# Kernel tuning notes

Measured on AMD Instinct MI355X. Metric: run time of the kernel, lower is better.

The kernel has to match this reference:

```python
import jax, jax.numpy as jnp
import numpy as np

D_MODEL = 1024
NUM_HEADS = 16
D_K = D_MODEL // NUM_HEADS


def setup_inputs() -> dict:
    key = jax.random.key(0)
    ks = jax.random.split(key, 9)
    B, S = 2, 2048
    s_in = 1.0 / np.sqrt(D_MODEL)
    x = jax.random.normal(ks[0], (B, S, D_MODEL), dtype=jnp.float32)
    # Linear weights stored as (in_features, out_features): y = x @ W + b
    Wq = jax.random.uniform(ks[1], (D_MODEL, D_MODEL), jnp.float32, -s_in, s_in)
    bq = jax.random.uniform(ks[2], (D_MODEL,), jnp.float32, -s_in, s_in)
    Wk = jax.random.uniform(ks[3], (D_MODEL, D_K), jnp.float32, -s_in, s_in)
    bk = jax.random.uniform(ks[4], (D_K,), jnp.float32, -s_in, s_in)
    Wv = jax.random.uniform(ks[5], (D_MODEL, D_K), jnp.float32, -s_in, s_in)
    bv = jax.random.uniform(ks[6], (D_K,), jnp.float32, -s_in, s_in)
    Wo = jax.random.uniform(ks[7], (D_MODEL, D_MODEL), jnp.float32, -s_in, s_in)
    bo = jax.random.uniform(ks[8], (D_MODEL,), jnp.float32, -s_in, s_in)
    return {"x": x, "Wq": Wq, "bq": bq, "Wk": Wk, "bk": bk,
            "Wv": Wv, "bv": bv, "Wo": Wo, "bo": bo}


def reference(x, Wq, bq, Wk, bk, Wv, bv, Wo, bo):
    B, S, _ = x.shape
    H, Dk = NUM_HEADS, D_K
    # Projections
    Q = (x @ Wq + bq).reshape(B, S, H, Dk).transpose(0, 2, 1, 3)  # [B,H,S,Dk]
    K = x @ Wk + bk                                               # [B,S,Dk] single KV head
    V = x @ Wv + bv                                               # [B,S,Dk]
    # Scores: query heads broadcast against the single shared KV head
    scores = jnp.einsum('bhqd,bkd->bhqk', Q, K) / jnp.sqrt(jnp.float32(Dk))
    attn = jax.nn.softmax(scores, axis=-1)                        # [B,H,S,S]
    out = jnp.einsum('bhqk,bkd->bhqd', attn, V)                   # [B,H,S,Dk]
    out = out.transpose(0, 2, 1, 3).reshape(B, S, H * Dk)         # [B,S,d_model]
    return out @ Wo + bo
```

## Files before the change

kernel.cpp:

```cpp
#include <hip/hip_runtime.h>
#include <hip/hip_bf16.h>

typedef __attribute__((ext_vector_type(8))) short bf16x8;
typedef __attribute__((ext_vector_type(4))) float f32x4;
typedef __attribute__((ext_vector_type(16))) float f32x16;
typedef __attribute__((ext_vector_type(4))) unsigned short ushort4v;

#define QSCALE 0.1803368801111204f

__device__ __forceinline__ unsigned short f2bf(float f) {
  union { float f; unsigned int u; } x; x.f = f;
  unsigned int u = x.u;
  unsigned int r = (u + 0x7fffu + ((u >> 16) & 1u)) >> 16;
  return (unsigned short)r;
}

__device__ __forceinline__ unsigned short cvt1bf(float a) {
  union { __hip_bfloat162 h; unsigned short s[2]; } c;
  c.h = __float22bfloat162_rn(make_float2(a, a));
  return c.s[0];
}

__device__ __forceinline__ void gll16(const unsigned short* g, unsigned short* l) {
  __builtin_amdgcn_global_load_lds(
      (const __attribute__((address_space(1))) unsigned int*)g,
      (__attribute__((address_space(3))) unsigned int*)l, 16, 0, 0);
}

__global__ __launch_bounds__(256) void prep_kernel(
    const float* __restrict__ x,
    const float* __restrict__ Wq, const float* __restrict__ Wk,
    const float* __restrict__ Wv, const float* __restrict__ Wo,
    unsigned short* __restrict__ xb,
    unsigned short* __restrict__ QKVt, unsigned short* __restrict__ Wot) {
  int z = blockIdx.z;
  if (z == 4) {
    size_t base = ((size_t)(blockIdx.y * 32 + blockIdx.x)) * 4096 + threadIdx.x * 16;
#pragma unroll
    for (int c = 0; c < 4; ++c) {
      float4 v = *(const float4*)(x + base + c * 4);
      ushort4v o = { f2bf(v.x), f2bf(v.y), f2bf(v.z), f2bf(v.w) };
      *(ushort4v*)(xb + base + c * 4) = o;
    }
    return;
  }
  __shared__ float t[32][33];
  const float* src;
  unsigned short* dst;
  int C, rowoff;
  if (z == 0)      { src = Wq; dst = QKVt; C = 1024; rowoff = 0; }
  else if (z == 1) { src = Wk; dst = QKVt; C = 64;   rowoff = 1024; }
  else if (z == 2) { src = Wv; dst = QKVt; C = 64;   rowoff = 1088; }
  else             { src = Wo; dst = Wot;  C = 1024; rowoff = 0; }
  int c0 = blockIdx.x * 32, r0 = blockIdx.y * 32;
  if (c0 >= C) return;
  int tx = threadIdx.x & 31, ty = threadIdx.x >> 5;
#pragma unroll
  for (int i = 0; i < 32; i += 8)
    t[ty + i][tx] = src[(size_t)(r0 + ty + i) * C + c0 + tx];
  __syncthreads();
#pragma unroll
  for (int i = 0; i < 32; i += 8)
    dst[(size_t)(rowoff + c0 + ty + i) * 1024 + r0 + tx] = f2bf(t[tx][ty + i]);
}

template <typename OutT, bool QKVMODE>
__global__ __launch_bounds__(256) void gemm_bf16_kernel(
    const unsigned short* __restrict__ A, const unsigned short* __restrict__ Bt,
    const float* __restrict__ b0, const float* __restrict__ b1,
    const float* __restrict__ b2, OutT* __restrict__ C,
    unsigned short* __restrict__ Vt, int M, int N, int K) {
  __shared__ __align__(16) unsigned short As[2][128 * 32];
  __shared__ __align__(16) unsigned short Bs[2][64 * 32];
  int tid = threadIdx.x;
  int wid = tid >> 6, lane = tid & 63;
  int l15 = lane & 15, quad = lane >> 4;
  int m0 = blockIdx.x * 128, n0 = blockIdx.y * 64;
  int mw = (wid >> 1) * 64, nw = (wid & 1) * 32;
  f32x4 acc[4][2];
#pragma unroll
  for (int i = 0; i < 4; i++)
#pragma unroll
    for (int j = 0; j < 2; j++)
#pragma unroll
      for (int e = 0; e < 4; ++e) acc[i][j][e] = 0.f;

  const unsigned short* Ag = A + (size_t)(m0 + (tid >> 2)) * K + (tid & 3) * 8;
  const unsigned short* Bg = Bt + (size_t)(n0 + (tid >> 2)) * K + (tid & 3) * 8;

  gll16(Ag, As[0] + tid * 8);
  gll16(Ag + (size_t)64 * K, As[0] + 2048 + tid * 8);
  gll16(Bg, Bs[0] + tid * 8);

  for (int k0 = 0; k0 < K; k0 += 32) {
    int cur = (k0 >> 5) & 1;
    if (k0 + 32 < K) {
      int nxt = cur ^ 1;
      gll16(Ag + k0 + 32, As[nxt] + tid * 8);
      gll16(Ag + (size_t)64 * K + k0 + 32, As[nxt] + 2048 + tid * 8);
      gll16(Bg + k0 + 32, Bs[nxt] + tid * 8);
      asm volatile("s_waitcnt vmcnt(3)" ::: "memory");
    } else {
      asm volatile("s_waitcnt vmcnt(0)" ::: "memory");
    }
    __builtin_amdgcn_s_barrier();
    __builtin_amdgcn_sched_barrier(0);
    const unsigned short* Asb = As[cur];
    const unsigned short* Bsb = Bs[cur];
    bf16x8 af[4], bfr[2];
#pragma unroll
    for (int t = 0; t < 4; ++t)
      af[t] = *(const bf16x8*)(Asb + (mw + t * 16 + l15) * 32 + quad * 8);
#pragma unroll
    for (int t = 0; t < 2; ++t)
      bfr[t] = *(const bf16x8*)(Bsb + (nw + t * 16 + l15) * 32 + quad * 8);
#pragma unroll
    for (int mt = 0; mt < 4; ++mt)
#pragma unroll
      for (int nt = 0; nt < 2; ++nt)
        acc[mt][nt] = __builtin_amdgcn_mfma_f32_16x16x32_bf16(
            af[mt], bfr[nt], acc[mt][nt], 0, 0, 0);
    asm volatile("s_waitcnt lgkmcnt(0)" ::: "memory");
    __builtin_amdgcn_sched_barrier(0);
    __builtin_amdgcn_s_barrier();
  }
#pragma unroll
  for (int mt = 0; mt < 4; ++mt)
#pragma unroll
    for (int nt = 0; nt < 2; ++nt) {
      int col = n0 + nw + nt * 16 + l15;
      float bias, cs;
      if constexpr (QKVMODE) {
        bias = (col < 1024) ? b0[col] : ((col < 1088) ? b1[col - 1024] : b2[col - 1088]);
        cs = (col < 1024) ? QSCALE : 1.0f;
      } else {
        bias = b0[col];
        cs = 1.0f;
      }
#pragma unroll
      for (int r = 0; r < 4; ++r) {
        int row = m0 + mw + mt * 16 + quad * 4 + r;
        float v = (acc[mt][nt][r] + bias) * cs;
        if constexpr (sizeof(OutT) == 2)
          C[(size_t)row * N + col] = f2bf(v);
        else
          C[(size_t)row * N + col] = v;
        if constexpr (QKVMODE) {
          if (col >= 1088)
            Vt[((size_t)(row >> 11) * 64 + (col - 1088)) * 2048 + (row & 2047)] =
                f2bf(v);
        }
      }
    }
}

__global__ __launch_bounds__(512, 4) void flash_attn_kernel(
    const unsigned short* __restrict__ QKV,
    const unsigned short* __restrict__ Vt,
    unsigned short* __restrict__ AO) {
  constexpr int S = 2048, LDQ = 1152;
  constexpr int PK = 72, PP = 72;
  __shared__ unsigned short Ks[2][64 * PK];
  __shared__ unsigned short Vs[2][64 * PK];
  __shared__ unsigned short Ps[8][32 * PP];
  int tid = threadIdx.x;
  int wid = tid >> 6, lane = tid & 63;
  int l31 = lane & 31, half = lane >> 5;
  int p = wid & 3, ks = wid >> 2;
  int q0 = blockIdx.x * 128, h = blockIdx.y, b = blockIdx.z;

  const unsigned short* Qb =
      QKV + (size_t)(b * S + q0 + p * 32 + l31) * LDQ + h * 64 + half * 8;
  bf16x8 qf[4];
#pragma unroll
  for (int f = 0; f < 4; ++f) qf[f] = *(const bf16x8*)(Qb + f * 16);

  int u = tid & 255, sl = tid >> 8;
  int srow = u >> 2, sc = (u & 3) * 8;
  const unsigned short* Kgb = QKV + ((size_t)b * S) * LDQ + 1024;
  const unsigned short* Vgb = Vt + ((size_t)(b * 64 + srow)) * 2048;

  f32x16 oa0, oa1;
#pragma unroll
  for (int r = 0; r < 16; ++r) { oa0[r] = 0.f; oa1[r] = 0.f; }
  float rs[16];
#pragma unroll
  for (int r = 0; r < 16; ++r) rs[r] = 0.f;

  int kb0 = sl * 1024;
  bf16x8 ka = *(const bf16x8*)(Kgb + (size_t)(kb0 + srow) * LDQ + sc);
  bf16x8 kc = *(const bf16x8*)(Kgb + (size_t)(kb0 + srow) * LDQ + sc + 32);
  bf16x8 va = *(const bf16x8*)(Vgb + kb0 + sc);
  bf16x8 vc = *(const bf16x8*)(Vgb + kb0 + sc + 32);

  unsigned short* Pw = Ps[wid];
  unsigned short* Ksb = Ks[ks];
  unsigned short* Vsb = Vs[ks];

  for (int kt = 0; kt < 16; ++kt) {
    *(bf16x8*)(Ks[sl] + srow * PK + sc) = ka;
    *(bf16x8*)(Ks[sl] + srow * PK + sc + 32) = kc;
    *(bf16x8*)(Vs[sl] + srow * PK + sc) = va;
    *(bf16x8*)(Vs[sl] + srow * PK + sc + 32) = vc;
    __syncthreads();
    if (kt + 1 < 16) {
      int kbn = sl * 1024 + (kt + 1) * 64;
      ka = *(const bf16x8*)(Kgb + (size_t)(kbn + srow) * LDQ + sc);
      kc = *(const bf16x8*)(Kgb + (size_t)(kbn + srow) * LDQ + sc + 32);
      va = *(const bf16x8*)(Vgb + kbn + sc);
      vc = *(const bf16x8*)(Vgb + kbn + sc + 32);
    }

#pragma unroll
    for (int n2 = 0; n2 < 2; ++n2) {
      f32x16 sacc;
#pragma unroll
      for (int i = 0; i < 16; ++i) sacc[i] = 0.f;
#pragma unroll
      for (int s = 0; s < 4; ++s) {
        bf16x8 kf =
            *(const bf16x8*)(Ksb + (n2 * 32 + l31) * PK + s * 16 + half * 8);
        sacc = __builtin_amdgcn_mfma_f32_32x32x16_bf16(qf[s], kf, sacc, 0, 0, 0);
      }
#pragma unroll
      for (int r = 0; r < 16; ++r) {
        float pr = __builtin_amdgcn_exp2f(sacc[r]);
        rs[r] += pr;
        int row = (r & 3) + 8 * (r >> 2) + 4 * half;
        Pw[row * PP + n2 * 32 + l31] = cvt1bf(pr);
      }
    }

    bf16x8 pf[4];
#pragma unroll
    for (int s = 0; s < 4; ++s)
      pf[s] = *(const bf16x8*)(Pw + l31 * PP + s * 16 + half * 8);
#pragma unroll
    for (int s = 0; s < 4; ++s) {
      bf16x8 vf0 = *(const bf16x8*)(Vsb + (l31)*PK + s * 16 + half * 8);
      bf16x8 vf1 = *(const bf16x8*)(Vsb + (32 + l31) * PK + s * 16 + half * 8);
      oa0 = __builtin_amdgcn_mfma_f32_32x32x16_bf16(pf[s], vf0, oa0, 0, 0, 0);
      oa1 = __builtin_amdgcn_mfma_f32_32x32x16_bf16(pf[s], vf1, oa1, 0, 0, 0);
    }
    __syncthreads();
  }

#pragma unroll
  for (int r = 0; r < 16; ++r) {
    float t = rs[r];
    t += __shfl_xor(t, 1, 32);
    t += __shfl_xor(t, 2, 32);
    t += __shfl_xor(t, 4, 32);
    t += __shfl_xor(t, 8, 32);
    t += __shfl_xor(t, 16, 32);
    rs[r] = t;
  }

  float* Cb = (float*)Ps;
  if (ks == 1) {
#pragma unroll
    for (int r = 0; r < 16; ++r) {
      int row = (r & 3) + 8 * (r >> 2) + 4 * half;
      Cb[(p * 32 + row) * 65 + l31] = oa0[r];
      Cb[(p * 32 + row) * 65 + 32 + l31] = oa1[r];
      if (l31 == 0) Cb[(p * 32 + row) * 65 + 64] = rs[r];
    }
  }
  __syncthreads();
  if (ks == 0) {
    unsigned short* Ob = AO + (size_t)(b * S + q0 + p * 32) * 1024 + h * 64;
#pragma unroll
    for (int r = 0; r < 16; ++r) {
      int row = (r & 3) + 8 * (r >> 2) + 4 * half;
      float p0 = Cb[(p * 32 + row) * 65 + l31];
      float p1 = Cb[(p * 32 + row) * 65 + 32 + l31];
      float rsu = Cb[(p * 32 + row) * 65 + 64];
      float inv = 1.0f / (rs[r] + rsu);
      Ob[(size_t)row * 1024 + l31] = f2bf((oa0[r] + p0) * inv);
      Ob[(size_t)row * 1024 + 32 + l31] = f2bf((oa1[r] + p1) * inv);
    }
  }
}

extern "C" void kernel_launch(void* const* d_in, const int* in_sizes, int n_in,
                              void* d_out, int out_size, void* d_ws, size_t ws_size,
                              hipStream_t stream) {
  const float* x  = (const float*)d_in[0];
  const float* Wq = (const float*)d_in[1];
  const float* bq = (const float*)d_in[2];
  const float* Wk = (const float*)d_in[3];
  const float* bk = (const float*)d_in[4];
  const float* Wv = (const float*)d_in[5];
  const float* bv = (const float*)d_in[6];
  const float* Wo = (const float*)d_in[7];
  const float* bo = (const float*)d_in[8];
  float* out = (float*)d_out;

  constexpr int B = 2, S = 2048, D = 1024, Dk = 64, H = 16;
  constexpr int M = B * S;
  constexpr int NQKV = D + 2 * Dk;

  char* ws = (char*)d_ws;
  unsigned short* xb   = (unsigned short*)ws; ws += (size_t)M * D * 2;
  unsigned short* QKVt = (unsigned short*)ws; ws += (size_t)NQKV * D * 2;
  unsigned short* Wot  = (unsigned short*)ws; ws += (size_t)D * D * 2;
  unsigned short* QKV  = (unsigned short*)ws; ws += (size_t)M * NQKV * 2;
  unsigned short* Vtb  = (unsigned short*)ws; ws += (size_t)B * Dk * S * 2;
  unsigned short* AO   = (unsigned short*)ws; ws += (size_t)M * D * 2;

  prep_kernel<<<dim3(32, 32, 5), 256, 0, stream>>>(x, Wq, Wk, Wv, Wo, xb, QKVt, Wot);

  gemm_bf16_kernel<unsigned short, true><<<dim3(M / 128, NQKV / 64), 256, 0, stream>>>(
      xb, QKVt, bq, bk, bv, QKV, Vtb, M, NQKV, D);

  flash_attn_kernel<<<dim3(S / 128, H, B), 512, 0, stream>>>(QKV, Vtb, AO);

  gemm_bf16_kernel<float, false><<<dim3(M / 128, D / 64), 256, 0, stream>>>(
      AO, Wot, bo, nullptr, nullptr, out, nullptr, M, D, D);
}
```

Baseline: 185.9 us.

## Triple-buffer GEMM with BK=64 and XOR-swizzled LDS layout

Reworks the projection GEMM main loop to stage K-tiles of 64 instead of 32, use three LDS buffers with a two-deep prefetch, and XOR-swizzle the LDS chunk layout to avoid bank conflicts on fragment reads. The aim is to hide more global-load latency and halve the barrier count per K. In exchange it raises LDS use to about 72KB per block, which may lower occupancy.

After: 192.6 us. 1.04x slower.

```diff
diff --git a/kernel.cpp b/kernel.cpp
--- a/kernel.cpp
+++ b/kernel.cpp
@@ -70,8 +70,8 @@
     const float* __restrict__ b0, const float* __restrict__ b1,
     const float* __restrict__ b2, OutT* __restrict__ C,
     unsigned short* __restrict__ Vt, int M, int N, int K) {
-  __shared__ __align__(16) unsigned short As[2][128 * 32];
-  __shared__ __align__(16) unsigned short Bs[2][64 * 32];
+  __shared__ __align__(16) unsigned short As[3][128 * 64];
+  __shared__ __align__(16) unsigned short Bs[3][64 * 64];
   int tid = threadIdx.x;
   int wid = tid >> 6, lane = tid & 63;
   int l15 = lane & 15, quad = lane >> 4;
@@ -85,21 +85,35 @@
 #pragma unroll
       for (int e = 0; e < 4; ++e) acc[i][j][e] = 0.f;
 
-  const unsigned short* Ag = A + (size_t)(m0 + (tid >> 2)) * K + (tid & 3) * 8;
-  const unsigned short* Bg = Bt + (size_t)(n0 + (tid >> 2)) * K + (tid & 3) * 8;
-
-  gll16(Ag, As[0] + tid * 8);
-  gll16(Ag + (size_t)64 * K, As[0] + 2048 + tid * 8);
-  gll16(Bg, Bs[0] + tid * 8);
-
-  for (int k0 = 0; k0 < K; k0 += 32) {
-    int cur = (k0 >> 5) & 1;
-    if (k0 + 32 < K) {
-      int nxt = cur ^ 1;
-      gll16(Ag + k0 + 32, As[nxt] + tid * 8);
-      gll16(Ag + (size_t)64 * K + k0 + 32, As[nxt] + 2048 + tid * 8);
-      gll16(Bg + k0 + 32, Bs[nxt] + tid * 8);
-      asm volatile("s_waitcnt vmcnt(3)" ::: "memory");
+  int srow = tid >> 3;
+  int schunk = (tid & 7) ^ (srow & 7);
+  const unsigned short* Ag = A + (size_t)(m0 + srow) * K + schunk * 8;
+  const unsigned short* Bg = Bt + (size_t)(n0 + srow) * K + schunk * 8;
+
+#define STAGE(buf, k0)                                        \
+  do {                                                        \
+    unsigned short* Ad = As[buf] + tid * 8;                   \
+    unsigned short* Bd = Bs[buf] + tid * 8;                   \
+    gll16(Ag + (k0), Ad);                                     \
+    gll16(Ag + (size_t)32 * K + (k0), Ad + 2048);             \
+    gll16(Ag + (size_t)64 * K + (k0), Ad + 4096);             \
+    gll16(Ag + (size_t)96 * K + (k0), Ad + 6144);             \
+    gll16(Bg + (k0), Bd);                                     \
+    gll16(Bg + (size_t)32 * K + (k0), Bd + 2048);             \
+  } while (0)
+
+  int nstep = K >> 6;
+  STAGE(0, 0);
+  if (nstep > 1) STAGE(1, 64);
+
+  int cur = 0;
+  for (int it = 0; it < nstep; ++it) {
+    if (it + 2 < nstep) {
+      int ib = (cur == 0) ? 2 : cur - 1;
+      STAGE(ib, (it + 2) * 64);
+      asm volatile("s_waitcnt vmcnt(12)" ::: "memory");
+    } else if (it + 1 < nstep) {
+      asm volatile("s_waitcnt vmcnt(6)" ::: "memory");
     } else {
       asm volatile("s_waitcnt vmcnt(0)" ::: "memory");
     }
@@ -107,23 +121,35 @@
     __builtin_amdgcn_sched_barrier(0);
     const unsigned short* Asb = As[cur];
     const unsigned short* Bsb = Bs[cur];
-    bf16x8 af[4], bfr[2];
-#pragma unroll
-    for (int t = 0; t < 4; ++t)
-      af[t] = *(const bf16x8*)(Asb + (mw + t * 16 + l15) * 32 + quad * 8);
-#pragma unroll
-    for (int t = 0; t < 2; ++t)
-      bfr[t] = *(const bf16x8*)(Bsb + (nw + t * 16 + l15) * 32 + quad * 8);
-#pragma unroll
-    for (int mt = 0; mt < 4; ++mt)
-#pragma unroll
-      for (int nt = 0; nt < 2; ++nt)
-        acc[mt][nt] = __builtin_amdgcn_mfma_f32_16x16x32_bf16(
-            af[mt], bfr[nt], acc[mt][nt], 0, 0, 0);
+#pragma unroll
+    for (int kk = 0; kk < 2; ++kk) {
+      bf16x8 af[4], bfr[2];
+#pragma unroll
+      for (int t = 0; t < 4; ++t) {
+        int row = mw + t * 16 + l15;
+        int off = (row * 64 + kk * 32 + quad * 8) ^ ((row & 7) << 3);
+        af[t] = *(const bf16x8*)(Asb + off);
+      }
+#pragma unroll
+      for (int t = 0; t < 2; ++t) {
+        int row = nw + t * 16 + l15;
+        int off = (row * 64 + kk * 32 + quad * 8) ^ ((row & 7) << 3);
+        bfr[t] = *(const bf16x8*)(Bsb + off);
+      }
+#pragma unroll
+      for (int mt = 0; mt < 4; ++mt)
+#pragma unroll
+        for (int nt = 0; nt < 2; ++nt)
+          acc[mt][nt] = __builtin_amdgcn_mfma_f32_16x16x32_bf16(
+              af[mt], bfr[nt], acc[mt][nt], 0, 0, 0);
+    }
     asm volatile("s_waitcnt lgkmcnt(0)" ::: "memory");
     __builtin_amdgcn_sched_barrier(0);
     __builtin_amdgcn_s_barrier();
-  }
+    cur = (cur == 2) ? 0 : cur + 1;
+  }
+#undef STAGE
+
 #pragma unroll
   for (int mt = 0; mt < 4; ++mt)
 #pragma unroll
```

## Keep attention probabilities in registers via transposed QK MFMA and permlane swap

Applied to the files above, without the earlier changes.

Computes S^T by swapping the MFMA operands, so each lane holds a query column's scores. The exponentiated probabilities are packed to bf16 with v_cvt_pk_bf16_f32 and rearranged with v_permlane32_swap into the A-operand layout for the PV MFMA. This removes the per-warp P shared-memory round trip and its LDS traffic, and shrinks LDS use, which may help occupancy. The row sum becomes a single scalar reduced with one cross-half shuffle, at the cost of inline asm that depends on gfx950 instructions.

Result: faster. 173.3 us (-6.8%).

```diff
diff --git a/kernel.cpp b/kernel.cpp
--- a/kernel.cpp
+++ b/kernel.cpp
@@ -13,12 +13,6 @@
   unsigned int u = x.u;
   unsigned int r = (u + 0x7fffu + ((u >> 16) & 1u)) >> 16;
   return (unsigned short)r;
-}
-
-__device__ __forceinline__ unsigned short cvt1bf(float a) {
-  union { __hip_bfloat162 h; unsigned short s[2]; } c;
-  c.h = __float22bfloat162_rn(make_float2(a, a));
-  return c.s[0];
 }
 
 __device__ __forceinline__ void gll16(const unsigned short* g, unsigned short* l) {
@@ -159,10 +153,8 @@
     const unsigned short* __restrict__ Vt,
     unsigned short* __restrict__ AO) {
   constexpr int S = 2048, LDQ = 1152;
-  constexpr int PK = 72, PP = 72;
-  __shared__ unsigned short Ks[2][64 * PK];
-  __shared__ unsigned short Vs[2][64 * PK];
-  __shared__ unsigned short Ps[8][32 * PP];
+  constexpr int PK = 72;
+  __shared__ __align__(16) unsigned short smem[2][2][64 * PK];
   int tid = threadIdx.x;
   int wid = tid >> 6, lane = tid & 63;
   int l31 = lane & 31, half = lane >> 5;
@@ -183,9 +175,7 @@
   f32x16 oa0, oa1;
 #pragma unroll
   for (int r = 0; r < 16; ++r) { oa0[r] = 0.f; oa1[r] = 0.f; }
-  float rs[16];
-#pragma unroll
-  for (int r = 0; r < 16; ++r) rs[r] = 0.f;
+  float rs = 0.f;
 
   int kb0 = sl * 1024;
   bf16x8 ka = *(const bf16x8*)(Kgb + (size_t)(kb0 + srow) * LDQ + sc);
@@ -193,15 +183,14 @@
   bf16x8 va = *(const bf16x8*)(Vgb + kb0 + sc);
   bf16x8 vc = *(const bf16x8*)(Vgb + kb0 + sc + 32);
 
-  unsigned short* Pw = Ps[wid];
-  unsigned short* Ksb = Ks[ks];
-  unsigned short* Vsb = Vs[ks];
+  unsigned short* Ksb = smem[ks][0];
+  unsigned short* Vsb = smem[ks][1];
 
   for (int kt = 0; kt < 16; ++kt) {
-    *(bf16x8*)(Ks[sl] + srow * PK + sc) = ka;
-    *(bf16x8*)(Ks[sl] + srow * PK + sc + 32) = kc;
-    *(bf16x8*)(Vs[sl] + srow * PK + sc) = va;
-    *(bf16x8*)(Vs[sl] + srow * PK + sc + 32) = vc;
+    *(bf16x8*)(smem[sl][0] + srow * PK + sc) = ka;
+    *(bf16x8*)(smem[sl][0] + srow * PK + sc + 32) = kc;
+    *(bf16x8*)(smem[sl][1] + srow * PK + sc) = va;
+    *(bf16x8*)(smem[sl][1] + srow * PK + sc + 32) = vc;
     __syncthreads();
     if (kt + 1 < 16) {
       int kbn = sl * 1024 + (kt + 1) * 64;
@@ -220,51 +209,48 @@
       for (int s = 0; s < 4; ++s) {
         bf16x8 kf =
             *(const bf16x8*)(Ksb + (n2 * 32 + l31) * PK + s * 16 + half * 8);
-        sacc = __builtin_amdgcn_mfma_f32_32x32x16_bf16(qf[s], kf, sacc, 0, 0, 0);
+        sacc = __builtin_amdgcn_mfma_f32_32x32x16_bf16(kf, qf[s], sacc, 0, 0, 0);
       }
 #pragma unroll
-      for (int r = 0; r < 16; ++r) {
-        float pr = __builtin_amdgcn_exp2f(sacc[r]);
-        rs[r] += pr;
-        int row = (r & 3) + 8 * (r >> 2) + 4 * half;
-        Pw[row * PP + n2 * 32 + l31] = cvt1bf(pr);
+      for (int t = 0; t < 2; ++t) {
+        float pr[8];
+#pragma unroll
+        for (int j = 0; j < 8; ++j) {
+          pr[j] = __builtin_amdgcn_exp2f(sacc[t * 8 + j]);
+          rs += pr[j];
+        }
+        unsigned w0A, w1A, w0B, w1B;
+        asm("v_cvt_pk_bf16_f32 %0, %1, %2" : "=v"(w0A) : "v"(pr[0]), "v"(pr[1]));
+        asm("v_cvt_pk_bf16_f32 %0, %1, %2" : "=v"(w1A) : "v"(pr[2]), "v"(pr[3]));
+        asm("v_cvt_pk_bf16_f32 %0, %1, %2" : "=v"(w0B) : "v"(pr[4]), "v"(pr[5]));
+        asm("v_cvt_pk_bf16_f32 %0, %1, %2" : "=v"(w1B) : "v"(pr[6]), "v"(pr[7]));
+        asm volatile("v_permlane32_swap_b32 %0, %1" : "+v"(w0A), "+v"(w0B));
+        asm volatile("v_permlane32_swap_b32 %0, %1" : "+v"(w1A), "+v"(w1B));
+        union { unsigned u[4]; bf16x8 v; } afu;
+        afu.u[0] = w0A; afu.u[1] = w1A; afu.u[2] = w0B; afu.u[3] = w1B;
+        int sg = n2 * 2 + t;
+        bf16x8 vf0 = *(const bf16x8*)(Vsb + (l31) * PK + sg * 16 + half * 8);
+        bf16x8 vf1 = *(const bf16x8*)(Vsb + (32 + l31) * PK + sg * 16 + half * 8);
+        oa0 = __builtin_amdgcn_mfma_f32_32x32x16_bf16(afu.v, vf0, oa0, 0, 0, 0);
+        oa1 = __builtin_amdgcn_mfma_f32_32x32x16_bf16(afu.v, vf1, oa1, 0, 0, 0);
       }
     }
-
-    bf16x8 pf[4];
-#pragma unroll
-    for (int s = 0; s < 4; ++s)
-      pf[s] = *(const bf16x8*)(Pw + l31 * PP + s * 16 + half * 8);
-#pragma unroll
-    for (int s = 0; s < 4; ++s) {
-      bf16x8 vf0 = *(const bf16x8*)(Vsb + (l31)*PK + s * 16 + half * 8);
-      bf16x8 vf1 = *(const bf16x8*)(Vsb + (32 + l31) * PK + s * 16 + half * 8);
-      oa0 = __builtin_amdgcn_mfma_f32_32x32x16_bf16(pf[s], vf0, oa0, 0, 0, 0);
-      oa1 = __builtin_amdgcn_mfma_f32_32x32x16_bf16(pf[s], vf1, oa1, 0, 0, 0);
-    }
     __syncthreads();
   }
 
-#pragma unroll
-  for (int r = 0; r < 16; ++r) {
-    float t = rs[r];
-    t += __shfl_xor(t, 1, 32);
-    t += __shfl_xor(t, 2, 32);
-    t += __shfl_xor(t, 4, 32);
-    t += __shfl_xor(t, 8, 32);
-    t += __shfl_xor(t, 16, 32);
-    rs[r] = t;
-  }
-
-  float* Cb = (float*)Ps;
+  float rsf = rs + __shfl_xor(rs, 32, 64);
+
+  float* Cb = (float*)smem;
   if (ks == 1) {
 #pragma unroll
     for (int r = 0; r < 16; ++r) {
       int row = (r & 3) + 8 * (r >> 2) + 4 * half;
-      Cb[(p * 32 + row) * 65 + l31] = oa0[r];
-      Cb[(p * 32 + row) * 65 + 32 + l31] = oa1[r];
-      if (l31 == 0) Cb[(p * 32 + row) * 65 + 64] = rs[r];
-    }
+      Cb[(p * 32 + row) * 66 + l31] = oa0[r];
+      Cb[(p * 32 + row) * 66 + 32 + l31] = oa1[r];
+    }
+    if (half == 0) Cb[(p * 32 + l31) * 66 + 64] = rsf;
+  } else {
+    if (half == 0) Cb[(p * 32 + l31) * 66 + 65] = rsf;
   }
   __syncthreads();
   if (ks == 0) {
@@ -272,10 +258,9 @@
 #pragma unroll
     for (int r = 0; r < 16; ++r) {
       int row = (r & 3) + 8 * (r >> 2) + 4 * half;
-      float p0 = Cb[(p * 32 + row) * 65 + l31];
-      float p1 = Cb[(p * 32 + row) * 65 + 32 + l31];
-      float rsu = Cb[(p * 32 + row) * 65 + 64];
-      float inv = 1.0f / (rs[r] + rsu);
+      float p0 = Cb[(p * 32 + row) * 66 + l31];
+      float p1 = Cb[(p * 32 + row) * 66 + 32 + l31];
+      float inv = 1.0f / (Cb[(p * 32 + row) * 66 + 64] + Cb[(p * 32 + row) * 66 + 65]);
       Ob[(size_t)row * 1024 + l31] = f2bf((oa0[r] + p0) * inv);
       Ob[(size_t)row * 1024 + 32 + l31] = f2bf((oa1[r] + p1) * inv);
     }
```
